# Optimization experiments

Measured on AMD Instinct MI355X. Metric: run time of the kernel, lower is better.

The kernel has to match this reference:

```python
import jax, jax.numpy as jnp
import numpy as np

B, S, H = 1024, 512, 768
D1, D2 = 128, 1


def setup_inputs() -> dict:
    key = jax.random.key(0)
    k_feat, k_start, k_len, k_w1, k_w2 = jax.random.split(key, 5)
    features_extract = jax.random.normal(k_feat, (B, S, H), dtype=jnp.float32)
    start_token_idx = jax.random.randint(k_start, (B,), 1, 200, dtype=jnp.int64)
    span_len = jax.random.randint(k_len, (B,), 1, 65, dtype=jnp.int64)
    end_token_idx = start_token_idx + span_len  # guaranteed start < end <= 264 < S
    W1 = jax.random.normal(k_w1, (2 * H, D1), dtype=jnp.float32) * (1.0 / np.sqrt(2 * H))
    b1 = jnp.zeros((D1,), dtype=jnp.float32)
    W2 = jax.random.normal(k_w2, (D1, D2), dtype=jnp.float32) * (1.0 / np.sqrt(D1))
    b2 = jnp.zeros((D2,), dtype=jnp.float32)
    return {
        "features_extract": features_extract,
        "start_token_idx": start_token_idx,
        "end_token_idx": end_token_idx,
        "W1": W1, "b1": b1, "W2": W2, "b2": b2,
    }


def reference(features_extract, start_token_idx, end_token_idx, W1, b1, W2, b2):
    # CLS feature: token 0 of each example -> [B, 1, H]
    features_cls = features_extract[:, 0, :][:, None, :]

    # Ragged span mean-pool (vectorized replacement for the per-example loop):
    # mask[b, s] = start[b] <= s < end[b]
    pos = jnp.arange(features_extract.shape[1])  # [S]
    mask = (pos[None, :] >= start_token_idx[:, None]) & (pos[None, :] < end_token_idx[:, None])
    maskf = mask.astype(features_extract.dtype)  # [B, S]
    span_sum = jnp.einsum('bsh,bs->bh', features_extract, maskf)
    span_len = (end_token_idx - start_token_idx).astype(features_extract.dtype)  # >= 1
    features_crc = (span_sum / span_len[:, None])[:, None, :]  # [B, 1, H]

    # Concat + MLP head (dropout layers are identity in eval)
    features = jnp.concatenate([features_cls, features_crc], axis=2)  # [B, 1, 2H]
    h = jax.nn.relu(jnp.einsum('bid,dk->bik', features, W1) + b1)
    out = jax.nn.sigmoid(jnp.einsum('bik,ko->bio', h, W2) + b2)  # [B, 1, 1]
    return out
```

## Files before the change

### kernel.cpp

```cpp
#include <hip/hip_runtime.h>
#include <math.h>

constexpr int Bn = 1024;
constexpr int S  = 512;
constexpr int H  = 768;
constexpr int D1 = 128;
constexpr int HV = H / 4;
constexpr int NH = 512;


__global__ __launch_bounds__(256) void fused_pool_clshead(
    const float* __restrict__ feat, const int* __restrict__ start,
    const int* __restrict__ endp, float* __restrict__ gp,
    const float* __restrict__ W1, float* __restrict__ P) {
  __shared__ float g[4][384];
  __shared__ float part[2][4][D1];

  const int t = threadIdx.x;

  if (blockIdx.x < NH) {
    const int c = blockIdx.x & 1;
    const int e0 = (blockIdx.x >> 1) * 4;
    const int dglob0 = c * 384;

    for (int i = t; i < 384; i += 256) {
      const int e = i / 96;
      const int j = i % 96;
      float4 v = *reinterpret_cast<const float4*>(
          feat + (size_t)(e0 + e) * S * H + dglob0 + j * 4);
      reinterpret_cast<float4*>(&g[e][0])[j] = v;
    }
    __syncthreads();

    const int k = t & (D1 - 1);
    const int sub = t >> 7;
    const int gofs = sub * 192;
    const float* Wc = W1 + (size_t)(dglob0 + gofs) * D1 + k;

    float a0 = 0.f, a1 = 0.f, a2 = 0.f, a3 = 0.f;
    #pragma unroll 4
    for (int d = 0; d < 192; d += 4) {
      float w0 = Wc[(size_t)(d + 0) * D1];
      float w1 = Wc[(size_t)(d + 1) * D1];
      float w2 = Wc[(size_t)(d + 2) * D1];
      float w3 = Wc[(size_t)(d + 3) * D1];
      float4 g0 = *reinterpret_cast<const float4*>(&g[0][gofs + d]);
      float4 g1 = *reinterpret_cast<const float4*>(&g[1][gofs + d]);
      float4 g2 = *reinterpret_cast<const float4*>(&g[2][gofs + d]);
      float4 g3 = *reinterpret_cast<const float4*>(&g[3][gofs + d]);
      a0 += g0.x * w0 + g0.y * w1 + g0.z * w2 + g0.w * w3;
      a1 += g1.x * w0 + g1.y * w1 + g1.z * w2 + g1.w * w3;
      a2 += g2.x * w0 + g2.y * w1 + g2.z * w2 + g2.w * w3;
      a3 += g3.x * w0 + g3.y * w1 + g3.z * w2 + g3.w * w3;
    }
    part[sub][0][k] = a0;
    part[sub][1][k] = a1;
    part[sub][2][k] = a2;
    part[sub][3][k] = a3;
    __syncthreads();

    if (t < D1) {
      #pragma unroll
      for (int e = 0; e < 4; ++e) {
        P[((size_t)c * Bn + (e0 + e)) * D1 + t] = part[0][e][t] + part[1][e][t];
      }
    }
    return;
  }

  if (t >= 192) return;
  const int bb = blockIdx.x - NH;
  const int b = bb >> 1;
  const int p = bb & 1;
  const float4* base = reinterpret_cast<const float4*>(feat) + (size_t)b * (S * HV);

  const int s0 = start[b];
  const int s1 = endp[b];
  float4 a0{0,0,0,0}, a1{0,0,0,0}, a2{0,0,0,0}, a3{0,0,0,0};
  int s = s0 + p;
  for (; s + 6 < s1; s += 8) {
    float4 v0 = base[(size_t)(s    ) * HV + t];
    float4 v1 = base[(size_t)(s + 2) * HV + t];
    float4 v2 = base[(size_t)(s + 4) * HV + t];
    float4 v3 = base[(size_t)(s + 6) * HV + t];
    a0.x += v0.x; a0.y += v0.y; a0.z += v0.z; a0.w += v0.w;
    a1.x += v1.x; a1.y += v1.y; a1.z += v1.z; a1.w += v1.w;
    a2.x += v2.x; a2.y += v2.y; a2.z += v2.z; a2.w += v2.w;
    a3.x += v3.x; a3.y += v3.y; a3.z += v3.z; a3.w += v3.w;
  }
  for (; s < s1; s += 2) {
    float4 v = base[(size_t)s * HV + t];
    a0.x += v.x; a0.y += v.y; a0.z += v.z; a0.w += v.w;
  }
  const float inv = 1.0f / (float)(s1 - s0);
  float4 r;
  r.x = ((a0.x + a1.x) + (a2.x + a3.x)) * inv;
  r.y = ((a0.y + a1.y) + (a2.y + a3.y)) * inv;
  r.z = ((a0.z + a1.z) + (a2.z + a3.z)) * inv;
  r.w = ((a0.w + a1.w) + (a2.w + a3.w)) * inv;
  reinterpret_cast<float4*>(gp)[((size_t)p * Bn + b) * HV + t] = r;
}

__global__ __launch_bounds__(256) void crc_head(
    const float* __restrict__ gp, const float* __restrict__ W1,
    float* __restrict__ P) {
  __shared__ float g[4][192];
  __shared__ float part[2][4][D1];

  const int t = threadIdx.x;
  const int cc = blockIdx.x & 3;
  const int e0 = (blockIdx.x >> 2) * 4;
  const int dd0 = cc * 192;

  for (int i = t; i < 192; i += 256) {
    const int e = i / 48;
    const int j = i % 48;
    const float* b0 = gp + (size_t)(e0 + e) * H + dd0;
    float4 u0 = reinterpret_cast<const float4*>(b0)[j];
    float4 u1 = reinterpret_cast<const float4*>(b0 + (size_t)Bn * H)[j];
    float4 v;
    v.x = u0.x + u1.x; v.y = u0.y + u1.y;
    v.z = u0.z + u1.z; v.w = u0.w + u1.w;
    reinterpret_cast<float4*>(&g[e][0])[j] = v;
  }
  __syncthreads();

  const int k = t & (D1 - 1);
  const int sub = t >> 7;
  const int gofs = sub * 96;
  const float* Wc = W1 + (size_t)(H + dd0 + gofs) * D1 + k;

  float a0 = 0.f, a1 = 0.f, a2 = 0.f, a3 = 0.f;
  #pragma unroll 4
  for (int d = 0; d < 96; d += 4) {
    float w0 = Wc[(size_t)(d + 0) * D1];
    float w1 = Wc[(size_t)(d + 1) * D1];
    float w2 = Wc[(size_t)(d + 2) * D1];
    float w3 = Wc[(size_t)(d + 3) * D1];
    float4 g0 = *reinterpret_cast<const float4*>(&g[0][gofs + d]);
    float4 g1 = *reinterpret_cast<const float4*>(&g[1][gofs + d]);
    float4 g2 = *reinterpret_cast<const float4*>(&g[2][gofs + d]);
    float4 g3 = *reinterpret_cast<const float4*>(&g[3][gofs + d]);
    a0 += g0.x * w0 + g0.y * w1 + g0.z * w2 + g0.w * w3;
    a1 += g1.x * w0 + g1.y * w1 + g1.z * w2 + g1.w * w3;
    a2 += g2.x * w0 + g2.y * w1 + g2.z * w2 + g2.w * w3;
    a3 += g3.x * w0 + g3.y * w1 + g3.z * w2 + g3.w * w3;
  }
  part[sub][0][k] = a0;
  part[sub][1][k] = a1;
  part[sub][2][k] = a2;
  part[sub][3][k] = a3;
  __syncthreads();

  if (t < D1) {
    #pragma unroll
    for (int e = 0; e < 4; ++e) {
      P[((size_t)(2 + cc) * Bn + (e0 + e)) * D1 + t] =
          part[0][e][t] + part[1][e][t];
    }
  }
}

__global__ __launch_bounds__(256) void finalize(
    const float* __restrict__ P, const float* __restrict__ b1,
    const float* __restrict__ W2, const float* __restrict__ b2,
    float* __restrict__ out) {
  const int t = threadIdx.x;
  const int w = t >> 6, l = t & 63;
  const int e = blockIdx.x * 4 + w;
  const int k0 = l, k1 = l + 64;
  float h0 = b1[k0], h1 = b1[k1];
  #pragma unroll
  for (int c = 0; c < 6; ++c) {
    h0 += P[((size_t)c * Bn + e) * D1 + k0];
    h1 += P[((size_t)c * Bn + e) * D1 + k1];
  }
  h0 = fmaxf(h0, 0.f); h1 = fmaxf(h1, 0.f);
  float v = h0 * W2[k0] + h1 * W2[k1];
  #pragma unroll
  for (int off = 32; off > 0; off >>= 1) v += __shfl_down(v, off);
  if (l == 0) out[e] = 1.0f / (1.0f + expf(-(v + b2[0])));
}

extern "C" void kernel_launch(void* const* d_in, const int* in_sizes, int n_in,
                              void* d_out, int out_size, void* d_ws, size_t ws_size,
                              hipStream_t stream) {
  const float* feat = (const float*)d_in[0];
  const int* start  = (const int*)d_in[1];
  const int* endp   = (const int*)d_in[2];
  const float* W1   = (const float*)d_in[3];
  const float* b1   = (const float*)d_in[4];
  const float* W2   = (const float*)d_in[5];
  const float* b2   = (const float*)d_in[6];
  float* out = (float*)d_out;

  float* wsf = (float*)d_ws;
  float* gp  = wsf;
  float* P   = gp + (size_t)2 * Bn * H;

  hipLaunchKernelGGL(fused_pool_clshead, dim3(NH + Bn * 2), dim3(256), 0,
                     stream, feat, start, endp, gp, W1, P);
  hipLaunchKernelGGL(crc_head, dim3(Bn), dim3(256), 0, stream, gp, W1, P);
  hipLaunchKernelGGL(finalize, dim3(Bn / 4), dim3(256), 0, stream,
                     P, b1, W2, b2, out);
}
```

Baseline: 33.96 us.

## Pool each span in one block with four waves and an in-block reduction

The span pooling used to run as two 192-thread blocks per example (even and odd rows), each writing a partial sum to global memory, and crc_head added the two partials back together. Now one 256-thread block handles each example: each of its four waves takes every fourth row across all 768 columns, and the waves combine their sums through shared memory before writing a single pooled vector. This halves the pooling block count, removes the extra partial-sum traffic and the extra add in crc_head, and lets all 256 threads load. The crc_head inner loop is also widened to 8 weights per iteration. The cost is a __syncthreads and shared-memory reduction per block, and fewer independent loads in flight per block on short spans.

```diff
diff --git a/kernel.cpp b/kernel.cpp
--- a/kernel.cpp
+++ b/kernel.cpp
@@ -13,12 +13,14 @@
     const float* __restrict__ feat, const int* __restrict__ start,
     const int* __restrict__ endp, float* __restrict__ gp,
     const float* __restrict__ W1, float* __restrict__ P) {
-  __shared__ float g[4][384];
-  __shared__ float part[2][4][D1];
+  __shared__ __align__(16) char smem[12288];
 
   const int t = threadIdx.x;
 
   if (blockIdx.x < NH) {
+    float (*g)[384] = reinterpret_cast<float (*)[384]>(smem);
+    float (*part)[4][D1] = reinterpret_cast<float (*)[4][D1]>(smem + 6144);
+
     const int c = blockIdx.x & 1;
     const int e0 = (blockIdx.x >> 1) * 4;
     const int dglob0 = c * 384;
@@ -68,37 +70,60 @@
     return;
   }
 
-  if (t >= 192) return;
-  const int bb = blockIdx.x - NH;
-  const int b = bb >> 1;
-  const int p = bb & 1;
-  const float4* base = reinterpret_cast<const float4*>(feat) + (size_t)b * (S * HV);
-
-  const int s0 = start[b];
-  const int s1 = endp[b];
-  float4 a0{0,0,0,0}, a1{0,0,0,0}, a2{0,0,0,0}, a3{0,0,0,0};
-  int s = s0 + p;
-  for (; s + 6 < s1; s += 8) {
-    float4 v0 = base[(size_t)(s    ) * HV + t];
-    float4 v1 = base[(size_t)(s + 2) * HV + t];
-    float4 v2 = base[(size_t)(s + 4) * HV + t];
-    float4 v3 = base[(size_t)(s + 6) * HV + t];
-    a0.x += v0.x; a0.y += v0.y; a0.z += v0.z; a0.w += v0.w;
-    a1.x += v1.x; a1.y += v1.y; a1.z += v1.z; a1.w += v1.w;
-    a2.x += v2.x; a2.y += v2.y; a2.z += v2.z; a2.w += v2.w;
-    a3.x += v3.x; a3.y += v3.y; a3.z += v3.z; a3.w += v3.w;
-  }
-  for (; s < s1; s += 2) {
-    float4 v = base[(size_t)s * HV + t];
-    a0.x += v.x; a0.y += v.y; a0.z += v.z; a0.w += v.w;
-  }
-  const float inv = 1.0f / (float)(s1 - s0);
-  float4 r;
-  r.x = ((a0.x + a1.x) + (a2.x + a3.x)) * inv;
-  r.y = ((a0.y + a1.y) + (a2.y + a3.y)) * inv;
-  r.z = ((a0.z + a1.z) + (a2.z + a3.z)) * inv;
-  r.w = ((a0.w + a1.w) + (a2.w + a3.w)) * inv;
-  reinterpret_cast<float4*>(gp)[((size_t)p * Bn + b) * HV + t] = r;
+  {
+    float4 (*pacc)[3][64] = reinterpret_cast<float4 (*)[3][64]>(smem);
+    const int b = blockIdx.x - NH;
+    const int w = t >> 6;
+    const int l = t & 63;
+    const float4* base =
+        reinterpret_cast<const float4*>(feat) + (size_t)b * (S * HV);
+
+    const int s0 = start[b];
+    const int s1 = endp[b];
+
+    float4 c0{0,0,0,0}, c1{0,0,0,0}, c2{0,0,0,0};
+    float4 d0{0,0,0,0}, d1{0,0,0,0}, d2{0,0,0,0};
+    int s = s0 + w;
+    for (; s + 4 < s1; s += 8) {
+      const float4* r0 = base + (size_t)s * HV;
+      const float4* r1 = base + (size_t)(s + 4) * HV;
+      float4 u0 = r0[l], u1 = r0[l + 64], u2 = r0[l + 128];
+      float4 v0 = r1[l], v1 = r1[l + 64], v2 = r1[l + 128];
+      c0.x += u0.x; c0.y += u0.y; c0.z += u0.z; c0.w += u0.w;
+      c1.x += u1.x; c1.y += u1.y; c1.z += u1.z; c1.w += u1.w;
+      c2.x += u2.x; c2.y += u2.y; c2.z += u2.z; c2.w += u2.w;
+      d0.x += v0.x; d0.y += v0.y; d0.z += v0.z; d0.w += v0.w;
+      d1.x += v1.x; d1.y += v1.y; d1.z += v1.z; d1.w += v1.w;
+      d2.x += v2.x; d2.y += v2.y; d2.z += v2.z; d2.w += v2.w;
+    }
+    for (; s < s1; s += 4) {
+      const float4* r0 = base + (size_t)s * HV;
+      float4 u0 = r0[l], u1 = r0[l + 64], u2 = r0[l + 128];
+      c0.x += u0.x; c0.y += u0.y; c0.z += u0.z; c0.w += u0.w;
+      c1.x += u1.x; c1.y += u1.y; c1.z += u1.z; c1.w += u1.w;
+      c2.x += u2.x; c2.y += u2.y; c2.z += u2.z; c2.w += u2.w;
+    }
+    c0.x += d0.x; c0.y += d0.y; c0.z += d0.z; c0.w += d0.w;
+    c1.x += d1.x; c1.y += d1.y; c1.z += d1.z; c1.w += d1.w;
+    c2.x += d2.x; c2.y += d2.y; c2.z += d2.z; c2.w += d2.w;
+    pacc[w][0][l] = c0;
+    pacc[w][1][l] = c1;
+    pacc[w][2][l] = c2;
+    __syncthreads();
+
+    if (t < 192) {
+      const int seg = t >> 6, ln = t & 63;
+      float4 a = pacc[0][seg][ln], bb = pacc[1][seg][ln];
+      float4 cq = pacc[2][seg][ln], dq = pacc[3][seg][ln];
+      const float inv = 1.0f / (float)(s1 - s0);
+      float4 r;
+      r.x = ((a.x + bb.x) + (cq.x + dq.x)) * inv;
+      r.y = ((a.y + bb.y) + (cq.y + dq.y)) * inv;
+      r.z = ((a.z + bb.z) + (cq.z + dq.z)) * inv;
+      r.w = ((a.w + bb.w) + (cq.w + dq.w)) * inv;
+      reinterpret_cast<float4*>(gp)[(size_t)b * HV + t] = r;
+    }
+  }
 }
 
 __global__ __launch_bounds__(256) void crc_head(
@@ -110,17 +135,12 @@
   const int t = threadIdx.x;
   const int cc = blockIdx.x & 3;
   const int e0 = (blockIdx.x >> 2) * 4;
-  const int dd0 = cc * 192;
-
-  for (int i = t; i < 192; i += 256) {
-    const int e = i / 48;
-    const int j = i % 48;
-    const float* b0 = gp + (size_t)(e0 + e) * H + dd0;
-    float4 u0 = reinterpret_cast<const float4*>(b0)[j];
-    float4 u1 = reinterpret_cast<const float4*>(b0 + (size_t)Bn * H)[j];
-    float4 v;
-    v.x = u0.x + u1.x; v.y = u0.y + u1.y;
-    v.z = u0.z + u1.z; v.w = u0.w + u1.w;
+  const int dd04 = cc * 48;
+
+  if (t < 192) {
+    const int e = t / 48;
+    const int j = t % 48;
+    float4 v = reinterpret_cast<const float4*>(gp)[(size_t)(e0 + e) * HV + dd04 + j];
     reinterpret_cast<float4*>(&g[e][0])[j] = v;
   }
   __syncthreads();
@@ -128,23 +148,28 @@
   const int k = t & (D1 - 1);
   const int sub = t >> 7;
   const int gofs = sub * 96;
-  const float* Wc = W1 + (size_t)(H + dd0 + gofs) * D1 + k;
+  const float* Wc = W1 + (size_t)(H + cc * 192 + gofs) * D1 + k;
 
   float a0 = 0.f, a1 = 0.f, a2 = 0.f, a3 = 0.f;
-  #pragma unroll 4
-  for (int d = 0; d < 96; d += 4) {
+  #pragma unroll 2
+  for (int d = 0; d < 96; d += 8) {
     float w0 = Wc[(size_t)(d + 0) * D1];
     float w1 = Wc[(size_t)(d + 1) * D1];
     float w2 = Wc[(size_t)(d + 2) * D1];
     float w3 = Wc[(size_t)(d + 3) * D1];
-    float4 g0 = *reinterpret_cast<const float4*>(&g[0][gofs + d]);
-    float4 g1 = *reinterpret_cast<const float4*>(&g[1][gofs + d]);
-    float4 g2 = *reinterpret_cast<const float4*>(&g[2][gofs + d]);
-    float4 g3 = *reinterpret_cast<const float4*>(&g[3][gofs + d]);
-    a0 += g0.x * w0 + g0.y * w1 + g0.z * w2 + g0.w * w3;
-    a1 += g1.x * w0 + g1.y * w1 + g1.z * w2 + g1.w * w3;
-    a2 += g2.x * w0 + g2.y * w1 + g2.z * w2 + g2.w * w3;
-    a3 += g3.x * w0 + g3.y * w1 + g3.z * w2 + g3.w * w3;
+    float w4 = Wc[(size_t)(d + 4) * D1];
+    float w5 = Wc[(size_t)(d + 5) * D1];
+    float w6 = Wc[(size_t)(d + 6) * D1];
+    float w7 = Wc[(size_t)(d + 7) * D1];
+    #define ACC8(i)                                                        \
+    {                                                                      \
+      float4 gA = *reinterpret_cast<const float4*>(&g[i][gofs + d]);       \
+      float4 gB = *reinterpret_cast<const float4*>(&g[i][gofs + d + 4]);   \
+      a##i += gA.x * w0 + gA.y * w1 + gA.z * w2 + gA.w * w3                \
+            + gB.x * w4 + gB.y * w5 + gB.z * w6 + gB.w * w7;               \
+    }
+    ACC8(0) ACC8(1) ACC8(2) ACC8(3)
+    #undef ACC8
   }
   part[sub][0][k] = a0;
   part[sub][1][k] = a1;
@@ -196,9 +221,9 @@
 
   float* wsf = (float*)d_ws;
   float* gp  = wsf;
-  float* P   = gp + (size_t)2 * Bn * H;
-
-  hipLaunchKernelGGL(fused_pool_clshead, dim3(NH + Bn * 2), dim3(256), 0,
+  float* P   = gp + (size_t)Bn * H;
+
+  hipLaunchKernelGGL(fused_pool_clshead, dim3(NH + Bn), dim3(256), 0,
                      stream, feat, start, endp, gp, W1, P);
   hipLaunchKernelGGL(crc_head, dim3(Bn), dim3(256), 0, stream, gp, W1, P);
   hipLaunchKernelGGL(finalize, dim3(Bn / 4), dim3(256), 0, stream,
```

Result: faster. 32.85 us (-3.3%).
